# Kernel tuning notes

Measured on AMD Instinct MI355X. Metric: run time of the kernel, lower is better.

## Reference

```python
import jax, jax.numpy as jnp
import numpy as np

B, S, D, H, M = 2, 2048, 1024, 16, 4096  # batch, seqlen, dim, n_heads, max_seq_len
HD = D // H  # head_dim = 64
EPS = 1e-5


def layernorm(x, g, b):
    mu = jnp.mean(x, axis=-1, keepdims=True)
    var = jnp.mean((x - mu) ** 2, axis=-1, keepdims=True)
    return (x - mu) * jax.lax.rsqrt(var + EPS) * g + b


def setup_inputs() -> dict:
    key = jax.random.key(0)
    ks = jax.random.split(key, 5)
    x = jax.random.normal(ks[0], (B, S, D), jnp.float32)
    # causal mask: >=0 -> keep, negative -> drop (forward does att *= mask >= 0)
    i = jnp.arange(S)
    mask = jnp.where(i[None, :] <= i[:, None], 0, -1).astype(jnp.int32)[None, None]
    w1 = jax.random.normal(ks[1], (4 * D, D), jnp.float32) * (D ** -0.5)
    b1 = jnp.zeros((4 * D,), jnp.float32)
    w2 = jax.random.normal(ks[2], (D, D), jnp.float32) * (D ** -0.5)
    b2 = jnp.zeros((D,), jnp.float32)
    g1 = jnp.ones((D,), jnp.float32)
    beta1 = jnp.zeros((D,), jnp.float32)
    g2 = jnp.ones((D,), jnp.float32)
    beta2 = jnp.zeros((D,), jnp.float32)
    pos_w = jax.random.normal(ks[3], (2 * M - 1,), jnp.float32) * 0.02
    return dict(x=x, mask=mask, w1=w1, b1=b1, w2=w2, b2=b2,
                g1=g1, beta1=beta1, g2=g2, beta2=beta2, pos_w=pos_w)


def reference(x, mask, w1, b1, w2, b2, g1, beta1, g2, beta2, pos_w):
    # f1 + silu, split into gate u and q/k/v
    h = jax.nn.silu(x @ w1.T + b1)                      # [B,S,4D]
    u, q, k, v = jnp.split(h, 4, axis=-1)
    to_heads = lambda t: t.reshape(B, S, H, HD).transpose(0, 2, 1, 3)  # [B,H,S,HD]
    u, q, k, v = map(to_heads, (u, q, k, v))
    # relative positional bias: bias[i,j] = pos_w[M-1 + (j - i)]
    rel = jnp.arange(S)[None, :] - jnp.arange(S)[:, None]
    bias = pos_w[M - 1 + rel]                           # [S,S]
    att = jax.nn.silu(jnp.einsum('bhqd,bhkd->bhqk', q, k) + bias)
    att = att * (mask >= 0)                             # [B,H,S,S]
    y = jnp.einsum('bhqk,bhkd->bhqd', att, v) * u
    y = y.transpose(0, 2, 1, 3).reshape(B, S, D)
    y = layernorm(y, g1, beta1)
    y = y @ w2.T + b2
    return layernorm(y + x, g2, beta2)
```

## Files before the change

kernel.cpp:

```cpp
#include <hip/hip_runtime.h>
#include <hip/hip_bf16.h>

#define BN   2
#define SEQ  2048
#define DIM  1024
#define NH   16
#define HD   64
#define D4   4096
#define MAXS 4096

using bf16 = __hip_bfloat16;
typedef __bf16 bf16x8 __attribute__((ext_vector_type(8)));
typedef float  f32x4  __attribute__((ext_vector_type(4)));
typedef unsigned short us8 __attribute__((ext_vector_type(8)));

__device__ __forceinline__ float bf2f(bf16 v){ return __bfloat162float(v); }
__device__ __forceinline__ bf16  f2bf(float v){ return __float2bfloat16(v); }
__device__ __forceinline__ float silu_f(float v){
  const float e = __expf(-v);
  return v * __builtin_amdgcn_rcpf(1.f + e);
}

__device__ __forceinline__ void async16(void* lds, const void* g){
  __builtin_amdgcn_global_load_lds((const __attribute__((address_space(1))) void*)g,
                                   (__attribute__((address_space(3))) void*)lds, 16, 0, 0);
}
__device__ __forceinline__ f32x4 mfma16(bf16x8 a, bf16x8 b, f32x4 c){
  return __builtin_amdgcn_mfma_f32_16x16x32_bf16(a, b, c, 0, 0, 0);
}

__global__ __launch_bounds__(256) void f2bk3(
    const float* __restrict__ a, bf16* __restrict__ ao, int na,
    const float* __restrict__ b, bf16* __restrict__ bo, int nb,
    const float* __restrict__ c, bf16* __restrict__ co)
{
  int i = (blockIdx.x * 256 + threadIdx.x) * 8;
  const float* in; bf16* out;
  if (i < na){ in = a; out = ao; }
  else if (i < na + nb){ in = b; out = bo; i -= na; }
  else { in = c; out = co; i -= na + nb; }
  const float4 v0 = *(const float4*)(in + i);
  const float4 v1 = *(const float4*)(in + i + 4);
  us8 o;
  bf16 t;
  t = f2bf(v0.x); o[0] = *(unsigned short*)&t;
  t = f2bf(v0.y); o[1] = *(unsigned short*)&t;
  t = f2bf(v0.z); o[2] = *(unsigned short*)&t;
  t = f2bf(v0.w); o[3] = *(unsigned short*)&t;
  t = f2bf(v1.x); o[4] = *(unsigned short*)&t;
  t = f2bf(v1.y); o[5] = *(unsigned short*)&t;
  t = f2bf(v1.z); o[6] = *(unsigned short*)&t;
  t = f2bf(v1.w); o[7] = *(unsigned short*)&t;
  *(us8*)((unsigned short*)out + i) = o;
}

template<int NTOT>
__global__ __launch_bounds__(512) void gemm_bt(
    const bf16* __restrict__ A, const bf16* __restrict__ W,
    const float* __restrict__ bias, bf16* __restrict__ outb, bf16* __restrict__ vt)
{
  constexpr int K = DIM;
  const int ntiles = NTOT / 128;
  const int m0 = (int)(blockIdx.x / ntiles) * 128;
  const int n0 = (int)(blockIdx.x % ntiles) * 128;
  __shared__ bf16 Al[2*128*32];
  __shared__ bf16 Bl[2*128*32];
  const int tid = threadIdx.x, wave = tid>>6, lane = tid&63;
  const int quad = lane>>4, l16 = lane&15;
  const int srow = lane>>2;
  const int sg   = ((lane&3) ^ ((lane>>3)&3)) * 8;
  const int wr = wave & 3, wc = wave >> 2;
  const int rkey = ((l16>>1)&3);

  f32x4 acc[2][4];
  #pragma unroll
  for (int i=0;i<2;i++)
    #pragma unroll
    for (int j=0;j<4;j++) acc[i][j] = (f32x4){0.f,0.f,0.f,0.f};

  const bf16* aB = A + m0*K;
  const bf16* wB = W + n0*K;

  for (int k0 = 0; k0 < K; k0 += 64){
    #pragma unroll
    for (int s=0;s<2;s++){
      const int kc = k0 + s*32;
      async16(&Al[s*4096 + wave*512], aB + (wave*16 + srow)*K + kc + sg);
      async16(&Bl[s*4096 + wave*512], wB + (wave*16 + srow)*K + kc + sg);
    }
    __syncthreads();
    #pragma unroll
    for (int s=0;s<2;s++){
      bf16x8 af[2], bv[4];
      #pragma unroll
      for (int mt=0;mt<2;mt++) af[mt] = *(const bf16x8*)&Al[s*4096 + (wr*32+mt*16+l16)*32 + (quad ^ rkey)*8];
      #pragma unroll
      for (int nt=0;nt<4;nt++) bv[nt] = *(const bf16x8*)&Bl[s*4096 + (wc*64+nt*16+l16)*32 + (quad ^ rkey)*8];
      #pragma unroll
      for (int mt=0;mt<2;mt++)
        #pragma unroll
        for (int nt=0;nt<4;nt++)
          acc[mt][nt] = mfma16(af[mt], bv[nt], acc[mt][nt]);
    }
    __syncthreads();
  }

  const bool vtile = (NTOT == 4096) && (n0 >= 3*DIM);
  if (!vtile){
    #pragma unroll
    for (int mt=0;mt<2;mt++){
      #pragma unroll
      for (int nt=0;nt<4;nt++){
        const int row = m0 + wr*32 + mt*16 + quad*4;
        const int col = n0 + wc*64 + nt*16 + l16;
        const float bvv = bias[col];
        #pragma unroll
        for (int r=0;r<4;r++){
          float v = silu_f(acc[mt][nt][r] + bvv);
          outb[(row+r)*NTOT + col] = f2bf(v);
        }
      }
    }
  } else {
    #pragma unroll
    for (int mt=0;mt<2;mt++){
      #pragma unroll
      for (int nt=0;nt<4;nt++){
        const int row = m0 + wr*32 + mt*16 + quad*4;
        const int colg = n0 + wc*64 + nt*16 + l16;
        const float bvv = bias[colg];
        const int col = colg - 3*DIM;
        const int hh = col >> 6, d = col & 63;
        const int bb = row >> 11, sl = row & 2047;
        ushort4 o;
        float v0 = silu_f(acc[mt][nt][0] + bvv);
        float v1 = silu_f(acc[mt][nt][1] + bvv);
        float v2 = silu_f(acc[mt][nt][2] + bvv);
        float v3 = silu_f(acc[mt][nt][3] + bvv);
        bf16 t0=f2bf(v0), t1=f2bf(v1), t2=f2bf(v2), t3=f2bf(v3);
        o.x=*(unsigned short*)&t0; o.y=*(unsigned short*)&t1;
        o.z=*(unsigned short*)&t2; o.w=*(unsigned short*)&t3;
        *(ushort4*)&vt[((bb*NH + hh)*HD + d)*SEQ + sl] = o;
      }
    }
  }
}

__global__ __launch_bounds__(256) void gemm_bt2(
    const bf16* __restrict__ A, const bf16* __restrict__ W,
    const float* __restrict__ bias, const float* __restrict__ resid,
    float* __restrict__ outf)
{
  constexpr int K = DIM, NTOT = DIM;
  const int ntiles = NTOT / 64;
  const int m0 = (int)(blockIdx.x / ntiles) * 128;
  const int n0 = (int)(blockIdx.x % ntiles) * 64;
  __shared__ bf16 Al[4*128*32];
  __shared__ bf16 Bl[4*64*32];
  const int tid = threadIdx.x, wave = tid>>6, lane = tid&63;
  const int quad = lane>>4, l16 = lane&15;
  const int srow = lane>>2;
  const int sg   = ((lane&3) ^ ((lane>>3)&3)) * 8;
  const int wm = wave*32;
  const int rkey = ((l16>>1)&3);

  f32x4 acc[2][4];
  #pragma unroll
  for (int i=0;i<2;i++)
    #pragma unroll
    for (int j=0;j<4;j++) acc[i][j] = (f32x4){0.f,0.f,0.f,0.f};

  const bf16* aB = A + m0*K;
  const bf16* wB = W + n0*K;

  for (int k0 = 0; k0 < K; k0 += 128){
    #pragma unroll
    for (int s=0;s<4;s++){
      const int kc = k0 + s*32;
      async16(&Al[s*4096 + wave*1024      ], aB + (wave*32      + srow)*K + kc + sg);
      async16(&Al[s*4096 + wave*1024 + 512], aB + (wave*32 + 16 + srow)*K + kc + sg);
      async16(&Bl[s*2048 + wave*512       ], wB + (wave*16      + srow)*K + kc + sg);
    }
    __syncthreads();
    #pragma unroll
    for (int s=0;s<4;s++){
      bf16x8 af[2], bv[4];
      #pragma unroll
      for (int mt=0;mt<2;mt++) af[mt] = *(const bf16x8*)&Al[s*4096 + (wm+mt*16+l16)*32 + (quad ^ rkey)*8];
      #pragma unroll
      for (int nt=0;nt<4;nt++) bv[nt] = *(const bf16x8*)&Bl[s*2048 + (nt*16+l16)*32 + (quad ^ rkey)*8];
      #pragma unroll
      for (int mt=0;mt<2;mt++)
        #pragma unroll
        for (int nt=0;nt<4;nt++)
          acc[mt][nt] = mfma16(af[mt], bv[nt], acc[mt][nt]);
    }
    __syncthreads();
  }

  #pragma unroll
  for (int mt=0;mt<2;mt++){
    #pragma unroll
    for (int nt=0;nt<4;nt++){
      const int row = m0 + wm + mt*16 + quad*4;
      const int col = n0 + nt*16 + l16;
      const float bvv = bias[col];
      #pragma unroll
      for (int r=0;r<4;r++){
        outf[(row+r)*NTOT + col] = acc[mt][nt][r] + bvv + resid[(row+r)*NTOT + col];
      }
    }
  }
}

__global__ __launch_bounds__(256) void attn(
    const bf16* __restrict__ h, const bf16* __restrict__ vt,
    const float* __restrict__ pw, bf16* __restrict__ y)
{
  const int bid = blockIdx.x;
  const int g  = bid & 31;
  const int qt = 31 - (bid >> 5);
  const int hh = g & 15, b = g >> 4;

  __shared__ __align__(16) char smem[16384 + 16384 + 17408 + 1024];
  bf16*  Kl  = (bf16*)smem;
  bf16*  Vl  = (bf16*)(smem + 16384);
  bf16*  Pl  = (bf16*)(smem + 32768);
  float* pwl = (float*)(smem + 50176);

  const int tid = threadIdx.x, wave = tid>>6, lane = tid&63;
  const int quad = lane>>4, l16 = lane&15;

  const bf16* kgb = h + b*SEQ*D4 + 2*DIM + hh*HD;
  const bf16* vgb = vt + (b*NH + hh)*HD*SEQ;
  const int krow8 = lane>>3;
  const int kgo   = ((lane&7) ^ krow8) * 8;
  const int vrow4 = lane>>4;

  const int q0 = qt * 64;

  const bf16* qbase = h + (b*SEQ + q0 + wave*16 + l16)*D4 + DIM + hh*HD;
  bf16x8 qf[2];
  qf[0] = *(const bf16x8*)(qbase + quad*8);
  qf[1] = *(const bf16x8*)(qbase + 32 + quad*8);

  f32x4 oacc[4];
  #pragma unroll
  for (int nt=0;nt<4;nt++) oacc[nt] = (f32x4){0.f,0.f,0.f,0.f};

  const int kmax = q0 + 64;

  bf16x8 kreg[4], vreg[4];
  float pv;
  #pragma unroll
  for (int t=0;t<4;t++)
    kreg[t] = *(const bf16x8*)(kgb + (wave*32 + t*8 + krow8)*D4 + kgo);
  #pragma unroll
  for (int t=0;t<4;t++){
    const int vg = ((lane&15) ^ (t*4 + vrow4)) * 8;
    vreg[t] = *(const bf16x8*)(vgb + (wave*16 + t*4 + vrow4)*SEQ + vg);
  }
  pv = pw[MAXS - 1 - q0 - 63 + tid];

  for (int k0 = 0; k0 < kmax; k0 += 128){
    __syncthreads();
    #pragma unroll
    for (int t=0;t<4;t++)
      *(bf16x8*)&Kl[(wave*32 + t*8)*64 + lane*8] = kreg[t];
    #pragma unroll
    for (int t=0;t<4;t++)
      *(bf16x8*)&Vl[(wave*16 + t*4)*128 + lane*8] = vreg[t];
    pwl[tid] = pv;
    __syncthreads();

    if (k0 + 128 < kmax){
      const int kn = k0 + 128;
      #pragma unroll
      for (int t=0;t<4;t++)
        kreg[t] = *(const bf16x8*)(kgb + (kn + wave*32 + t*8 + krow8)*D4 + kgo);
      #pragma unroll
      for (int t=0;t<4;t++){
        const int vg = ((lane&15) ^ (t*4 + vrow4)) * 8;
        vreg[t] = *(const bf16x8*)(vgb + (wave*16 + t*4 + vrow4)*SEQ + kn + vg);
      }
      pv = pw[MAXS - 1 + kn - q0 - 63 + tid];
    }

    f32x4 sacc[8];
    #pragma unroll
    for (int nt=0;nt<8;nt++) sacc[nt] = (f32x4){0.f,0.f,0.f,0.f};
    __builtin_amdgcn_s_setprio(1);
    #pragma unroll
    for (int ks=0;ks<2;ks++){
      #pragma unroll
      for (int nt=0;nt<8;nt++){
        bf16x8 kf = *(const bf16x8*)&Kl[(nt*16 + l16)*64 + ((ks*4 + quad) ^ (l16&7))*8];
        sacc[nt] = mfma16(kf, qf[ks], sacc[nt]);
      }
    }
    __builtin_amdgcn_s_setprio(0);

    bf16* Plw = Pl + wave*(16*136);
    const int dq = q0 - k0;
    const int qrl = wave*16 + l16;
    if (dq >= 127){
      #pragma unroll
      for (int nt=0;nt<8;nt++){
        const int kb = nt*16 + quad*4;
        ushort4 o; bf16 tb[4];
        #pragma unroll
        for (int r=0;r<4;r++){
          const int d = kb + r - qrl;
          const float bias = pwl[d + 63];
          tb[r] = f2bf(silu_f(sacc[nt][r] + bias));
        }
        o.x=*(unsigned short*)&tb[0]; o.y=*(unsigned short*)&tb[1];
        o.z=*(unsigned short*)&tb[2]; o.w=*(unsigned short*)&tb[3];
        *(ushort4*)&Plw[l16*136 + kb] = o;
      }
    } else {
      #pragma unroll
      for (int nt=0;nt<8;nt++){
        const int kb = nt*16 + quad*4;
        ushort4 o; bf16 tb[4];
        #pragma unroll
        for (int r=0;r<4;r++){
          const int d = kb + r - qrl;
          const float bias = pwl[d + 63];
          const float sv = silu_f(sacc[nt][r] + bias);
          tb[r] = f2bf((d <= dq) ? sv : 0.f);
        }
        o.x=*(unsigned short*)&tb[0]; o.y=*(unsigned short*)&tb[1];
        o.z=*(unsigned short*)&tb[2]; o.w=*(unsigned short*)&tb[3];
        *(ushort4*)&Plw[l16*136 + kb] = o;
      }
    }

    __builtin_amdgcn_s_setprio(1);
    #pragma unroll
    for (int ks=0;ks<4;ks++){
      bf16x8 pf = *(const bf16x8*)&Plw[l16*136 + ks*32 + quad*8];
      #pragma unroll
      for (int nt=0;nt<4;nt++){
        bf16x8 vf = *(const bf16x8*)&Vl[(nt*16 + l16)*128 + ((ks*4 + quad) ^ l16)*8];
        oacc[nt] = mfma16(pf, vf, oacc[nt]);
      }
    }
    __builtin_amdgcn_s_setprio(0);
  }

  const int qrow = q0 + wave*16 + quad*4;
  #pragma unroll
  for (int nt=0;nt<4;nt++){
    const int c = hh*HD + nt*16 + l16;
    #pragma unroll
    for (int r=0;r<4;r++){
      const int srow = b*SEQ + qrow + r;
      const float uu = bf2f(h[srow*D4 + c]);
      y[srow*DIM + c] = f2bf(oacc[nt][r] * uu);
    }
  }
}


template<bool FP32>
__global__ __launch_bounds__(256) void lnorm(const void* __restrict__ in,
    const float* __restrict__ g, const float* __restrict__ be, void* __restrict__ out)
{
  const int wave = threadIdx.x>>6, lane = threadIdx.x&63;
  const int row = blockIdx.x*4 + wave;
  float v[16];
  if (FP32){
    const float* p = (const float*)in + row*DIM;
    #pragma unroll
    for (int j=0;j<4;j++){
      const float4 t = *(const float4*)(p + j*256 + lane*4);
      v[j*4+0]=t.x; v[j*4+1]=t.y; v[j*4+2]=t.z; v[j*4+3]=t.w;
    }
  } else {
    const unsigned short* p = (const unsigned short*)in + row*DIM;
    #pragma unroll
    for (int j=0;j<2;j++){
      const us8 t = *(const us8*)(p + j*512 + lane*8);
      #pragma unroll
      for (int k=0;k<8;k++){
        unsigned short u = t[k];
        v[j*8+k] = bf2f(*(bf16*)&u);
      }
    }
  }
  float s = 0.f, ss = 0.f;
  #pragma unroll
  for (int e=0;e<16;e++){ s += v[e]; ss += v[e]*v[e]; }
  #pragma unroll
  for (int off=1; off<64; off<<=1){
    s  += __shfl_xor(s, off);
    ss += __shfl_xor(ss, off);
  }
  const float mu   = s * (1.f/DIM);
  const float var  = ss * (1.f/DIM) - mu*mu;
  const float rstd = rsqrtf(var + 1e-5f);
  if (FP32){
    float* q = (float*)out + row*DIM;
    #pragma unroll
    for (int j=0;j<4;j++){
      const int c = j*256 + lane*4;
      const float4 gv = *(const float4*)(g + c);
      const float4 bv = *(const float4*)(be + c);
      float4 o;
      o.x = (v[j*4+0]-mu)*rstd*gv.x + bv.x;
      o.y = (v[j*4+1]-mu)*rstd*gv.y + bv.y;
      o.z = (v[j*4+2]-mu)*rstd*gv.z + bv.z;
      o.w = (v[j*4+3]-mu)*rstd*gv.w + bv.w;
      *(float4*)(q + c) = o;
    }
  } else {
    unsigned short* q = (unsigned short*)out + row*DIM;
    #pragma unroll
    for (int j=0;j<2;j++){
      const int c = j*512 + lane*8;
      us8 o;
      #pragma unroll
      for (int k=0;k<8;k++){
        const float ov = (v[j*8+k]-mu)*rstd*g[c+k] + be[c+k];
        bf16 t = f2bf(ov);
        o[k] = *(unsigned short*)&t;
      }
      *(us8*)(q + c) = o;
    }
  }
}

extern "C" void kernel_launch(void* const* d_in, const int* in_sizes, int n_in,
                              void* d_out, int out_size, void* d_ws, size_t ws_size,
                              hipStream_t stream)
{
  const float* x   = (const float*)d_in[0];
  const float* w1  = (const float*)d_in[2];
  const float* b1  = (const float*)d_in[3];
  const float* w2  = (const float*)d_in[4];
  const float* b2  = (const float*)d_in[5];
  const float* g1  = (const float*)d_in[6];
  const float* be1 = (const float*)d_in[7];
  const float* g2  = (const float*)d_in[8];
  const float* be2 = (const float*)d_in[9];
  const float* pw  = (const float*)d_in[10];

  char* ws = (char*)d_ws;
  bf16*  h   = (bf16*)(ws);
  bf16*  vt  = (bf16*)(ws + (32u<<20));
  bf16*  y   = (bf16*)(ws + (40u<<20));
  bf16*  xb  = (bf16*)(ws + (48u<<20));
  bf16*  w1b = (bf16*)(ws + (56u<<20));
  bf16*  w2b = (bf16*)(ws + (64u<<20));
  bf16*  l1  = (bf16*)(ws + (66u<<20));
  float* z   = (float*)(ws + (74u<<20));

  const int NX  = BN*SEQ*DIM;
  const int NW1 = 4*DIM*DIM;
  const int NW2 = DIM*DIM;
  f2bk3<<<dim3((NX+NW1+NW2)/2048), dim3(256), 0, stream>>>(x, xb, NX, w1, w1b, NW1, w2, w2b);

  gemm_bt<4096><<<dim3(1024), dim3(512), 0, stream>>>(xb, w1b, b1, h, vt);
  attn<<<dim3(1024), dim3(256), 0, stream>>>(h, vt, pw, y);
  lnorm<false><<<dim3(1024), dim3(256), 0, stream>>>(y, g1, be1, l1);
  gemm_bt2<<<dim3(512), dim3(256), 0, stream>>>(l1, w2b, b2, x, z);
  lnorm<true><<<dim3(1024), dim3(256), 0, stream>>>(z, g2, be2, d_out);
}
```

Before: 225.2 us.

## Use async LDS loads, shrink P buffer, reorder query tiles in attention

Replaces the register-prefetched K/V double-staging with direct global-to-LDS async loads issued at the start of each iteration. This drops the software prefetch. The P tile is now written and consumed in 32-key chunks, so the per-wave P buffer shrinks from 16x136 to 16x40 and LDS use falls, which could raise occupancy. The query-tile order per block group is also changed to interleave long and short causal tiles for load balance. The cost is that load latency is no longer hidden behind the previous tile's compute.

```diff
diff --git a/kernel.cpp b/kernel.cpp
--- a/kernel.cpp
+++ b/kernel.cpp
@@ -219,14 +219,15 @@
 {
   const int bid = blockIdx.x;
   const int g  = bid & 31;
-  const int qt = 31 - (bid >> 5);
+  const int j  = bid >> 5, jp = j & 7, jq = j >> 3;
+  const int qt = (jq==0) ? 31-jp : (jq==1) ? 16+jp : (jq==2) ? 15-jp : jp;
   const int hh = g & 15, b = g >> 4;
 
-  __shared__ __align__(16) char smem[16384 + 16384 + 17408 + 1024];
+  __shared__ __align__(16) char smem[16384 + 16384 + 5120 + 1024];
   bf16*  Kl  = (bf16*)smem;
   bf16*  Vl  = (bf16*)(smem + 16384);
   bf16*  Pl  = (bf16*)(smem + 32768);
-  float* pwl = (float*)(smem + 50176);
+  float* pwl = (float*)(smem + 32768 + 5120);
 
   const int tid = threadIdx.x, wave = tid>>6, lane = tid&63;
   const int quad = lane>>4, l16 = lane&15;
@@ -250,41 +251,18 @@
 
   const int kmax = q0 + 64;
 
-  bf16x8 kreg[4], vreg[4];
-  float pv;
-  #pragma unroll
-  for (int t=0;t<4;t++)
-    kreg[t] = *(const bf16x8*)(kgb + (wave*32 + t*8 + krow8)*D4 + kgo);
-  #pragma unroll
-  for (int t=0;t<4;t++){
-    const int vg = ((lane&15) ^ (t*4 + vrow4)) * 8;
-    vreg[t] = *(const bf16x8*)(vgb + (wave*16 + t*4 + vrow4)*SEQ + vg);
-  }
-  pv = pw[MAXS - 1 - q0 - 63 + tid];
-
   for (int k0 = 0; k0 < kmax; k0 += 128){
     __syncthreads();
     #pragma unroll
     for (int t=0;t<4;t++)
-      *(bf16x8*)&Kl[(wave*32 + t*8)*64 + lane*8] = kreg[t];
-    #pragma unroll
-    for (int t=0;t<4;t++)
-      *(bf16x8*)&Vl[(wave*16 + t*4)*128 + lane*8] = vreg[t];
-    pwl[tid] = pv;
-    __syncthreads();
-
-    if (k0 + 128 < kmax){
-      const int kn = k0 + 128;
-      #pragma unroll
-      for (int t=0;t<4;t++)
-        kreg[t] = *(const bf16x8*)(kgb + (kn + wave*32 + t*8 + krow8)*D4 + kgo);
-      #pragma unroll
-      for (int t=0;t<4;t++){
-        const int vg = ((lane&15) ^ (t*4 + vrow4)) * 8;
-        vreg[t] = *(const bf16x8*)(vgb + (wave*16 + t*4 + vrow4)*SEQ + kn + vg);
-      }
-      pv = pw[MAXS - 1 + kn - q0 - 63 + tid];
-    }
+      async16(&Kl[(wave*32 + t*8)*64], kgb + (k0 + wave*32 + t*8 + krow8)*D4 + kgo);
+    #pragma unroll
+    for (int t=0;t<4;t++){
+      const int vg = ((lane&15) ^ (t*4 + vrow4)) * 8;
+      async16(&Vl[(wave*16 + t*4)*128], vgb + (wave*16 + t*4 + vrow4)*SEQ + k0 + vg);
+    }
+    pwl[tid] = pw[MAXS - 1 + k0 - q0 - 63 + tid];
+    __syncthreads();
 
     f32x4 sacc[8];
     #pragma unroll
@@ -300,53 +278,54 @@
     }
     __builtin_amdgcn_s_setprio(0);
 
-    bf16* Plw = Pl + wave*(16*136);
+    bf16* Plw = Pl + wave*(16*40);
     const int dq = q0 - k0;
     const int qrl = wave*16 + l16;
-    if (dq >= 127){
-      #pragma unroll
-      for (int nt=0;nt<8;nt++){
-        const int kb = nt*16 + quad*4;
-        ushort4 o; bf16 tb[4];
+    #pragma unroll
+    for (int hf=0; hf<4; hf++){
+      if (dq >= 127){
         #pragma unroll
-        for (int r=0;r<4;r++){
-          const int d = kb + r - qrl;
-          const float bias = pwl[d + 63];
-          tb[r] = f2bf(silu_f(sacc[nt][r] + bias));
+        for (int ntl=0; ntl<2; ntl++){
+          const int nt = hf*2 + ntl;
+          const int kb = nt*16 + quad*4;
+          ushort4 o; bf16 tb[4];
+          #pragma unroll
+          for (int r=0;r<4;r++){
+            const int d = kb + r - qrl;
+            const float bias = pwl[d + 63];
+            tb[r] = f2bf(silu_f(sacc[nt][r] + bias));
+          }
+          o.x=*(unsigned short*)&tb[0]; o.y=*(unsigned short*)&tb[1];
+          o.z=*(unsigned short*)&tb[2]; o.w=*(unsigned short*)&tb[3];
+          *(ushort4*)&Plw[l16*40 + ntl*16 + quad*4] = o;
         }
-        o.x=*(unsigned short*)&tb[0]; o.y=*(unsigned short*)&tb[1];
-        o.z=*(unsigned short*)&tb[2]; o.w=*(unsigned short*)&tb[3];
-        *(ushort4*)&Plw[l16*136 + kb] = o;
-      }
-    } else {
-      #pragma unroll
-      for (int nt=0;nt<8;nt++){
-        const int kb = nt*16 + quad*4;
-        ushort4 o; bf16 tb[4];
+      } else {
         #pragma unroll
-        for (int r=0;r<4;r++){
-          const int d = kb + r - qrl;
-          const float bias = pwl[d + 63];
-          const float sv = silu_f(sacc[nt][r] + bias);
-          tb[r] = f2bf((d <= dq) ? sv : 0.f);
+        for (int ntl=0; ntl<2; ntl++){
+          const int nt = hf*2 + ntl;
+          const int kb = nt*16 + quad*4;
+          ushort4 o; bf16 tb[4];
+          #pragma unroll
+          for (int r=0;r<4;r++){
+            const int d = kb + r - qrl;
+            const float bias = pwl[d + 63];
+            const float sv = silu_f(sacc[nt][r] + bias);
+            tb[r] = f2bf((d <= dq) ? sv : 0.f);
+          }
+          o.x=*(unsigned short*)&tb[0]; o.y=*(unsigned short*)&tb[1];
+          o.z=*(unsigned short*)&tb[2]; o.w=*(unsigned short*)&tb[3];
+          *(ushort4*)&Plw[l16*40 + ntl*16 + quad*4] = o;
         }
-        o.x=*(unsigned short*)&tb[0]; o.y=*(unsigned short*)&tb[1];
-        o.z=*(unsigned short*)&tb[2]; o.w=*(unsigned short*)&tb[3];
-        *(ushort4*)&Plw[l16*136 + kb] = o;
-      }
-    }
-
-    __builtin_amdgcn_s_setprio(1);
-    #pragma unroll
-    for (int ks=0;ks<4;ks++){
-      bf16x8 pf = *(const bf16x8*)&Plw[l16*136 + ks*32 + quad*8];
+      }
+      __builtin_amdgcn_s_setprio(1);
+      bf16x8 pf = *(const bf16x8*)&Plw[l16*40 + quad*8];
       #pragma unroll
       for (int nt=0;nt<4;nt++){
-        bf16x8 vf = *(const bf16x8*)&Vl[(nt*16 + l16)*128 + ((ks*4 + quad) ^ l16)*8];
+        bf16x8 vf = *(const bf16x8*)&Vl[(nt*16 + l16)*128 + ((hf*4 + quad) ^ l16)*8];
         oacc[nt] = mfma16(pf, vf, oacc[nt]);
       }
-    }
-    __builtin_amdgcn_s_setprio(0);
+      __builtin_amdgcn_s_setprio(0);
+    }
   }
 
   const int qrow = q0 + wave*16 + quad*4;
```

New measurement: 232.7 us. +3.3%, slower.
